# Kernel tuning notes

Hardware: AMD Instinct MI355X
Metric: run time of the kernel (lower is better)

The kernel has to match this reference:

```python
import jax, jax.numpy as jnp
import numpy as np

V_NUM = 4
NUM_HEADS = 8


def setup_inputs() -> dict:
    key = jax.random.key(0)
    k1, k2, k3 = jax.random.split(key, 3)
    B, C, H, W = 8, 512, 24, 24
    x = jax.random.normal(k1, (B, C, H, W), dtype=jnp.float32)
    # 1x1 conv weights stored as [out_ch, in_ch]
    w_qkv = jax.random.normal(k2, (3 * C, C), dtype=jnp.float32) * (C ** -0.5)
    w_proj = jax.random.normal(k3, (C, C), dtype=jnp.float32) * (C ** -0.5)
    b_proj = jnp.zeros((C,), dtype=jnp.float32)
    return {"x": x, "w_qkv": w_qkv, "w_proj": w_proj, "b_proj": b_proj}


def reference(x, w_qkv, w_proj, b_proj):
    B, C, H, W = x.shape
    hd = C // NUM_HEADS          # head dim
    scale = hd ** -0.5
    g = B // V_NUM               # batch groups
    N = V_NUM * H * W            # tokens per group

    # 1x1 conv qkv (no bias): [B, 3C, H, W]
    qkv = jnp.einsum('bchw,oc->bohw', x, w_qkv)
    # [g, v, 3C, H, W] -> [g, 3C, v, H, W] -> [g, heads, 3*hd, N]
    t = qkv.reshape(g, V_NUM, 3 * C, H, W).transpose(0, 2, 1, 3, 4)
    t = t.reshape(g, NUM_HEADS, 3 * hd, N)
    q, k, v = jnp.split(t, 3, axis=2)  # each [g, heads, hd, N]

    # attn = k^T @ q * scale : [g, heads, N, N]
    attn = jnp.einsum('ghdn,ghdm->ghnm', k, q) * scale
    attn = jax.nn.softmax(attn, axis=-2)  # softmax over the k axis (dim=-2)

    # out = v @ attn : [g, heads, hd, N]
    out = jnp.einsum('ghdn,ghnm->ghdm', v, attn)
    # [g, C, v, H, W] -> [g, v, C, H, W] -> [B, C, H, W]
    out = out.reshape(g, C, V_NUM, H, W).transpose(0, 2, 1, 3, 4).reshape(B, C, H, W)

    # 1x1 conv proj with bias
    out = jnp.einsum('bchw,oc->bohw', out, w_proj) + b_proj[None, :, None, None]
    return out
```

## Files before the change

kernel.cpp:

```cpp
#include <hip/hip_runtime.h>
#include <stdint.h>

typedef _Float16 f16;
typedef _Float16 half8 __attribute__((ext_vector_type(8)));
typedef _Float16 half4 __attribute__((ext_vector_type(4)));
typedef float floatx4 __attribute__((ext_vector_type(4)));

#define LOG2E 1.44269504088896340736f

__device__ __forceinline__ void async_cp16(const void* g, void* l) {
  __builtin_amdgcn_global_load_lds((const __attribute__((address_space(1))) void*)g,
                                   (__attribute__((address_space(3))) void*)l, 16, 0, 0);
}

__global__ __launch_bounds__(256) void k_prep(const float* __restrict__ x,
                                              f16* __restrict__ XT,
                                              const float* __restrict__ wqkv,
                                              const float* __restrict__ wproj,
                                              f16* __restrict__ WQ, f16* __restrict__ WP) {
  __shared__ f16 sT[64][72];
  const int bid = blockIdx.x;
  const int tid = threadIdx.x;
  if (bid < 576) {
    const int hw0 = (bid % 9) * 64, c0 = ((bid / 9) & 7) * 64, b = bid / 72;
    const int cc = tid >> 6, hwc = tid & 63;
    const float* xb = x + (size_t)b * 294912;
    for (int i = 0; i < 16; ++i) {
      int c = c0 + i * 4 + cc;
      sT[hwc][i * 4 + cc] = (f16)xb[c * 576 + hw0 + hwc];
    }
    __syncthreads();
    const int c_c = tid & 63, rr = tid >> 6;
    f16* xtb = XT + ((size_t)b * 576 + hw0) * 512 + c0;
    for (int j = 0; j < 16; ++j) {
      int r = j * 4 + rr;
      xtb[(size_t)r * 512 + c_c] = sT[r][c_c];
    }
  } else {
    const float SCALE_Q = 0.125f * LOG2E;
    const int total1 = 1536 * 512, total2 = 512 * 512;
    for (int idx = (bid - 576) * 256 + tid; idx < total1 + total2; idx += 128 * 256) {
      if (idx < total1) {
        int row = idx >> 9;
        float v = wqkv[idx];
        if ((row % 192) < 64) v *= SCALE_Q;
        WQ[idx] = (f16)v;
      } else {
        WP[idx - total1] = (f16)wproj[idx - total1];
      }
    }
  }
}

__global__ __launch_bounds__(256) void k_qkv_gemm(const f16* __restrict__ XT,
                                                  const f16* __restrict__ WQ,
                                                  f16* __restrict__ Qh, f16* __restrict__ Kh,
                                                  f16* __restrict__ Vh) {
  const int t0 = blockIdx.x * 128, n0 = blockIdx.y * 128;
  __shared__ alignas(16) f16 smem[2 * 128 * 64];
  f16* sA = smem;
  f16* sB = smem + 128 * 64;
  const int tid = threadIdx.x;
  const int wave = tid >> 6, lane = tid & 63, quad = lane >> 4, l16 = lane & 15;
  const int msub = (wave & 1) * 64, nsub = (wave >> 1) * 64;
  const floatx4 fzero = {0.f, 0.f, 0.f, 0.f};
  floatx4 acc[4][4];
  for (int i = 0; i < 4; ++i)
    for (int j = 0; j < 4; ++j) acc[i][j] = fzero;

  for (int k0 = 0; k0 < 512; k0 += 64) {
    __syncthreads();
    for (int p = 0; p < 4; ++p) {
      int e = p * 256 + tid;
      int row = e >> 3, colb = e & 7;
      async_cp16((const char*)XT + ((size_t)(t0 + row) * 512 + k0 + colb * 8) * 2,
                 (char*)sA + e * 16);
      async_cp16((const char*)WQ + ((size_t)(n0 + row) * 512 + k0 + colb * 8) * 2,
                 (char*)sB + e * 16);
    }
    __syncthreads();
    for (int f = 0; f < 2; ++f) {
      half8 a[4], bfr[4];
      for (int ms = 0; ms < 4; ++ms)
        a[ms] = *(const half8*)&sA[(msub + ms * 16 + l16) * 64 + f * 32 + quad * 8];
      for (int ns = 0; ns < 4; ++ns)
        bfr[ns] = *(const half8*)&sB[(nsub + ns * 16 + l16) * 64 + f * 32 + quad * 8];
      for (int ms = 0; ms < 4; ++ms)
        for (int ns = 0; ns < 4; ++ns)
          acc[ms][ns] =
              __builtin_amdgcn_mfma_f32_16x16x32_f16(a[ms], bfr[ns], acc[ms][ns], 0, 0, 0);
    }
  }
  for (int ms = 0; ms < 4; ++ms) {
    int tbase = t0 + msub + ms * 16 + quad * 4;
    for (int ns = 0; ns < 4; ++ns) {
      int row = n0 + nsub + ns * 16 + l16;
      int h = row / 192, rr2 = row % 192;
      int sel = rr2 >> 6, d = rr2 & 63;
      if (sel == 2) continue;
      for (int r = 0; r < 4; ++r) {
        int t = tbase + r;
        int b = t / 576, hw = t % 576;
        int g = b >> 2, v = b & 3;
        int n = v * 576 + hw;
        int gh = g * 8 + h;
        f16 hv = (f16)acc[ms][ns][r];
        size_t idx = ((size_t)gh * 2304 + n) * 64 + d;
        if (sel == 0)
          Qh[idx] = hv;
        else
          Kh[idx] = hv;
      }
    }
  }
  const int r0 = n0 % 192;
  if (r0 != 0) {
    const int vloc = (r0 == 128) ? 0 : 64;
    const int h = (n0 + vloc) / 192;
    f16* sVT = smem;
    __syncthreads();
    if ((wave >> 1) == (vloc >> 6)) {
      for (int ms = 0; ms < 4; ++ms) {
        int tok = msub + ms * 16 + quad * 4;
        for (int ns = 0; ns < 4; ++ns) {
          int d = ns * 16 + l16;
          half4 hv;
          for (int r = 0; r < 4; ++r) hv[r] = (f16)acc[ms][ns][r];
          *(half4*)&sVT[d * 136 + tok] = hv;
        }
      }
    }
    __syncthreads();
    for (int pss = 0; pss < 4; ++pss) {
      int d = pss * 16 + (tid >> 4), chunk = tid & 15;
      int t = t0 + chunk * 8;
      int b = t / 576, hw = t - b * 576;
      int gh = (b >> 2) * 8 + h, n = (b & 3) * 576 + hw;
      *(half8*)(Vh + (size_t)gh * 147456 + (size_t)d * 2304 + n) =
          *(const half8*)&sVT[d * 136 + chunk * 8];
    }
  }
}

__global__ __launch_bounds__(256) void k_attn(const f16* __restrict__ Qh,
                                              const f16* __restrict__ Kh,
                                              const f16* __restrict__ Vh,
                                              f16* __restrict__ AOT) {
  const int mt = blockIdx.x, gh = blockIdx.y;
  const int m0 = mt * 64;
  const int g = gh >> 3, h = gh & 7;
  const f16* Qg = Qh + (size_t)gh * 147456;
  const f16* Kg = Kh + (size_t)gh * 147456;
  const f16* Vg = Vh + (size_t)gh * 147456;
  __shared__ alignas(16) f16 sK[2][2][64 * 64];
  __shared__ alignas(16) f16 sV[2][2][64 * 64];
  const int tid = threadIdx.x;
  const int wave = tid >> 6, lane = tid & 63, quad = lane >> 4, l16 = lane & 15;
  const int wq = wave & 1, half = wave >> 1;
  const floatx4 fzero = {0.f, 0.f, 0.f, 0.f};
  const int sw = l16 & 7;

  auto stage_kv = [&](int ktile, int buf) {
#pragma unroll
    for (int p = 0; p < 8; ++p) {
      const int half_t = (p >> 1) & 1, isV = p >> 2;
      int idx = (p & 1) * 256 + tid;
      int row = idx >> 3, cb = idx & 7, sc = ((cb ^ (row & 7)) << 3);
      int nb = half_t * 1152 + ktile * 64;
      if (!isV)
        async_cp16(Kg + (size_t)(nb + row) * 64 + sc, (char*)&sK[half_t][buf][0] + idx * 16);
      else
        async_cp16(Vg + (size_t)row * 2304 + nb + sc, (char*)&sV[half_t][buf][0] + idx * 16);
    }
  };

  half8 qa[2][2];
  for (int s = 0; s < 2; ++s) {
    int qrow = m0 + wq * 32 + s * 16 + l16;
    qa[s][0] = *(const half8*)(Qg + (size_t)qrow * 64 + quad * 8);
    qa[s][1] = *(const half8*)(Qg + (size_t)qrow * 64 + 32 + quad * 8);
  }

  stage_kv(0, 0);
  __syncthreads();
  stage_kv(1, 1);

  float l_lane[2] = {0.f, 0.f};
  floatx4 o[2][4];
  for (int s = 0; s < 2; ++s)
    for (int dt = 0; dt < 4; ++dt) o[s][dt] = fzero;

  for (int kt = 0; kt < 18; ++kt) {
    const f16* bK = &sK[half][kt & 1][0];
    const f16* bV = &sV[half][kt & 1][0];

    half4 pf[2][4];
#pragma unroll
    for (int nt = 0; nt < 4; ++nt) {
      int krow = nt * 16 + l16;
      half8 kb0 = *(const half8*)&bK[krow * 64 + ((quad ^ sw) << 3)];
      half8 kb1 = *(const half8*)&bK[krow * 64 + (((4 + quad) ^ sw) << 3)];
#pragma unroll
      for (int s = 0; s < 2; ++s) {
        floatx4 t = __builtin_amdgcn_mfma_f32_16x16x32_f16(kb0, qa[s][0], fzero, 0, 0, 0);
        t = __builtin_amdgcn_mfma_f32_16x16x32_f16(kb1, qa[s][1], t, 0, 0, 0);
#pragma unroll
        for (int r = 0; r < 4; ++r) {
          float e = __builtin_amdgcn_exp2f(t[r]);
          l_lane[s] += e;
          pf[s][nt][r] = (f16)e;
        }
      }
    }
#pragma unroll
    for (int dt = 0; dt < 4; ++dt) {
      int vrow = dt * 16 + l16;
#pragma unroll
      for (int nt = 0; nt < 4; ++nt) {
        int chunk = nt * 2 + (quad >> 1);
        half4 vb = *(const half4*)&bV[vrow * 64 + ((chunk ^ sw) << 3) + (quad & 1) * 4];
#pragma unroll
        for (int s = 0; s < 2; ++s)
          o[s][dt] = __builtin_amdgcn_mfma_f32_16x16x16f16(pf[s][nt], vb, o[s][dt], 0, 0, 0);
      }
    }

    if (kt < 17) {
      __syncthreads();
      if (kt + 2 < 18) stage_kv(kt + 2, kt & 1);
    }
  }

  __syncthreads();
  float* cO = (float*)sK;
  float* cL = (float*)sV;
  if (half == 1) {
    for (int s = 0; s < 2; ++s) {
      cL[(wq * 2 + s) * 64 + lane] = l_lane[s];
      for (int dt = 0; dt < 4; ++dt)
        *(floatx4*)&cO[((((wq * 2 + s) * 4 + dt) * 64 + lane) * 4)] = o[s][dt];
    }
  }
  __syncthreads();
  if (half == 0) {
    for (int s = 0; s < 2; ++s) {
      l_lane[s] += cL[(wq * 2 + s) * 64 + lane];
      for (int dt = 0; dt < 4; ++dt)
        o[s][dt] += *(const floatx4*)&cO[((((wq * 2 + s) * 4 + dt) * 64 + lane) * 4)];
    }
    for (int s = 0; s < 2; ++s) {
      l_lane[s] += __shfl_xor(l_lane[s], 16, 64);
      l_lane[s] += __shfl_xor(l_lane[s], 32, 64);
      float inv[4];
      for (int r = 0; r < 4; ++r) {
        float lr = __shfl(l_lane[s], quad * 4 + r, 64);
        inv[r] = 1.f / lr;
      }
      for (int dt = 0; dt < 4; ++dt)
        for (int r = 0; r < 4; ++r) {
          int n_tok = m0 + wq * 32 + s * 16 + quad * 4 + r;
          int v = n_tok / 576, hw = n_tok % 576;
          int bb = g * 4 + v;
          int c = h * 64 + dt * 16 + l16;
          AOT[((size_t)bb * 576 + hw) * 512 + c] = (f16)(o[s][dt][r] * inv[r]);
        }
    }
  }
}

__global__ __launch_bounds__(256) void k_proj_gemm(const f16* __restrict__ AOT,
                                                   const f16* __restrict__ WP,
                                                   const float* __restrict__ bias,
                                                   float* __restrict__ out) {
  const int o0 = blockIdx.x * 64, t0 = blockIdx.y * 128;
  __shared__ alignas(16) f16 sA[64 * 64];
  __shared__ alignas(16) f16 sB[128 * 64];
  const int tid = threadIdx.x;
  const int wave = tid >> 6, lane = tid & 63, quad = lane >> 4, l16 = lane & 15;
  const int msub = (wave & 1) * 32, nsub = (wave >> 1) * 64;
  const floatx4 fzero = {0.f, 0.f, 0.f, 0.f};
  floatx4 acc[2][4];
  for (int i = 0; i < 2; ++i)
    for (int j = 0; j < 4; ++j) acc[i][j] = fzero;

  for (int k0 = 0; k0 < 512; k0 += 64) {
    __syncthreads();
    for (int p = 0; p < 2; ++p) {
      int e = p * 256 + tid;
      int row = e >> 3, colb = e & 7;
      async_cp16((const char*)WP + ((size_t)(o0 + row) * 512 + k0 + colb * 8) * 2,
                 (char*)sA + e * 16);
    }
    for (int p = 0; p < 4; ++p) {
      int e = p * 256 + tid;
      int row = e >> 3, colb = e & 7;
      async_cp16((const char*)AOT + ((size_t)(t0 + row) * 512 + k0 + colb * 8) * 2,
                 (char*)sB + e * 16);
    }
    __syncthreads();
    for (int f = 0; f < 2; ++f) {
      half8 a[2], bfr[4];
      for (int ms = 0; ms < 2; ++ms)
        a[ms] = *(const half8*)&sA[(msub + ms * 16 + l16) * 64 + f * 32 + quad * 8];
      for (int ns = 0; ns < 4; ++ns)
        bfr[ns] = *(const half8*)&sB[(nsub + ns * 16 + l16) * 64 + f * 32 + quad * 8];
      for (int ms = 0; ms < 2; ++ms)
        for (int ns = 0; ns < 4; ++ns)
          acc[ms][ns] =
              __builtin_amdgcn_mfma_f32_16x16x32_f16(a[ms], bfr[ns], acc[ms][ns], 0, 0, 0);
    }
  }
  for (int ms = 0; ms < 2; ++ms) {
    int o_row = o0 + msub + ms * 16 + quad * 4;
    for (int ns = 0; ns < 4; ++ns) {
      int t = t0 + nsub + ns * 16 + l16;
      int b = t / 576, hw = t % 576;
      for (int r = 0; r < 4; ++r) {
        int orow = o_row + r;
        out[(size_t)b * 294912 + (size_t)orow * 576 + hw] = acc[ms][ns][r] + bias[orow];
      }
    }
  }
}

extern "C" void kernel_launch(void* const* d_in, const int* in_sizes, int n_in,
                              void* d_out, int out_size, void* d_ws, size_t ws_size,
                              hipStream_t stream) {
  const float* x = (const float*)d_in[0];
  const float* wqkv = (const float*)d_in[1];
  const float* wproj = (const float*)d_in[2];
  const float* bias = (const float*)d_in[3];
  float* out = (float*)d_out;
  char* ws = (char*)d_ws;
  f16* XT = (f16*)(ws + 0);
  f16* WQ = (f16*)(ws + 4718592);
  f16* WP = (f16*)(ws + 6291456);
  f16* Qh = (f16*)(ws + 6815744);
  f16* Kh = (f16*)(ws + 11534336);
  f16* Vh = (f16*)(ws + 16252928);
  f16* AOT = (f16*)(ws + 20971520);

  k_prep<<<dim3(704), dim3(256), 0, stream>>>(x, XT, wqkv, wproj, WQ, WP);
  k_qkv_gemm<<<dim3(36, 12), dim3(256), 0, stream>>>(XT, WQ, Qh, Kh, Vh);
  k_attn<<<dim3(36, 16), dim3(256), 0, stream>>>(Qh, Kh, Vh, AOT);
  k_proj_gemm<<<dim3(8, 36), dim3(256), 0, stream>>>(AOT, WP, bias, out);
}
```

Before: 154.9 us.

## Split attention key range across blocks with global partials and reduction kernel

```diff
diff --git a/kernel.cpp b/kernel.cpp
--- a/kernel.cpp
+++ b/kernel.cpp
@@ -142,6 +142,139 @@
   }
 }
 
+__global__ __launch_bounds__(128) void k_attn_part(const f16* __restrict__ Qh,
+                                                   const f16* __restrict__ Kh,
+                                                   const f16* __restrict__ Vh,
+                                                   float* __restrict__ Opart,
+                                                   float* __restrict__ Lpart) {
+  const int mt = blockIdx.x, gh = blockIdx.y, ks = blockIdx.z;
+  const int m0 = mt * 64;
+  const f16* Qg = Qh + (size_t)gh * 147456;
+  const f16* Kg = Kh + (size_t)gh * 147456 + (size_t)ks * 73728;
+  const f16* Vg = Vh + (size_t)gh * 147456 + ks * 1152;
+  __shared__ alignas(16) f16 sK[2][64 * 64];
+  __shared__ alignas(16) f16 sV[2][64 * 64];
+  const int tid = threadIdx.x;
+  const int wave = tid >> 6, lane = tid & 63, quad = lane >> 4, l16 = lane & 15;
+  const floatx4 fzero = {0.f, 0.f, 0.f, 0.f};
+  const int sw = l16 & 7;
+
+  auto stage_kv = [&](int ktile, int buf) {
+    const int nb = ktile * 64;
+#pragma unroll
+    for (int p = 0; p < 4; ++p) {
+      int idx = p * 128 + tid;
+      int row = idx >> 3, cb = idx & 7, sc = ((cb ^ (row & 7)) << 3);
+      async_cp16(Kg + (size_t)(nb + row) * 64 + sc, (char*)&sK[buf][0] + idx * 16);
+    }
+#pragma unroll
+    for (int p = 0; p < 4; ++p) {
+      int idx = p * 128 + tid;
+      int row = idx >> 3, cb = idx & 7, sc = ((cb ^ (row & 7)) << 3);
+      async_cp16(Vg + (size_t)row * 2304 + nb + sc, (char*)&sV[buf][0] + idx * 16);
+    }
+  };
+
+  half8 qa[2][2];
+  for (int s = 0; s < 2; ++s) {
+    int qrow = m0 + wave * 32 + s * 16 + l16;
+    qa[s][0] = *(const half8*)(Qg + (size_t)qrow * 64 + quad * 8);
+    qa[s][1] = *(const half8*)(Qg + (size_t)qrow * 64 + 32 + quad * 8);
+  }
+
+  stage_kv(0, 0);
+  __syncthreads();
+  stage_kv(1, 1);
+
+  float l_lane[2] = {0.f, 0.f};
+  floatx4 o[2][4];
+  for (int s = 0; s < 2; ++s)
+    for (int dt = 0; dt < 4; ++dt) o[s][dt] = fzero;
+
+  for (int kt = 0; kt < 18; ++kt) {
+    const f16* bK = &sK[kt & 1][0];
+    const f16* bV = &sV[kt & 1][0];
+
+    half4 pf[2][4];
+#pragma unroll
+    for (int nt = 0; nt < 4; ++nt) {
+      int krow = nt * 16 + l16;
+      half8 kb0 = *(const half8*)&bK[krow * 64 + ((quad ^ sw) << 3)];
+      half8 kb1 = *(const half8*)&bK[krow * 64 + (((4 + quad) ^ sw) << 3)];
+#pragma unroll
+      for (int s = 0; s < 2; ++s) {
+        floatx4 t = __builtin_amdgcn_mfma_f32_16x16x32_f16(kb0, qa[s][0], fzero, 0, 0, 0);
+        t = __builtin_amdgcn_mfma_f32_16x16x32_f16(kb1, qa[s][1], t, 0, 0, 0);
+#pragma unroll
+        for (int r = 0; r < 4; ++r) {
+          float e = __builtin_amdgcn_exp2f(t[r]);
+          l_lane[s] += e;
+          pf[s][nt][r] = (f16)e;
+        }
+      }
+    }
+#pragma unroll
+    for (int dt = 0; dt < 4; ++dt) {
+      int vrow = dt * 16 + l16;
+#pragma unroll
+      for (int nt = 0; nt < 4; ++nt) {
+        int chunk = nt * 2 + (quad >> 1);
+        half4 vb = *(const half4*)&bV[vrow * 64 + ((chunk ^ sw) << 3) + (quad & 1) * 4];
+#pragma unroll
+        for (int s = 0; s < 2; ++s)
+          o[s][dt] = __builtin_amdgcn_mfma_f32_16x16x16f16(pf[s][nt], vb, o[s][dt], 0, 0, 0);
+      }
+    }
+
+    if (kt < 17) {
+      __syncthreads();
+      if (kt + 2 < 18) stage_kv(kt + 2, kt & 1);
+    }
+  }
+
+  const size_t slice = (size_t)(ks * 16 + gh);
+  for (int s = 0; s < 2; ++s) {
+    l_lane[s] += __shfl_xor(l_lane[s], 16, 64);
+    l_lane[s] += __shfl_xor(l_lane[s], 32, 64);
+    if (quad == 0)
+      Lpart[slice * 2304 + m0 + wave * 32 + s * 16 + l16] = l_lane[s];
+  }
+  float* Ob = Opart + slice * (2304 * 64);
+  for (int s = 0; s < 2; ++s)
+    for (int dt = 0; dt < 4; ++dt)
+      for (int r = 0; r < 4; ++r) {
+        int q = m0 + wave * 32 + s * 16 + quad * 4 + r;
+        Ob[(size_t)q * 64 + dt * 16 + l16] = o[s][dt][r];
+      }
+}
+
+__global__ __launch_bounds__(256) void k_attn_red(const float* __restrict__ Opart,
+                                                  const float* __restrict__ Lpart,
+                                                  f16* __restrict__ AOT) {
+  const int mt = blockIdx.x, gh = blockIdx.y;
+  const int g = gh >> 3, h = gh & 7;
+  const int tid = threadIdx.x;
+  const int q = mt * 64 + (tid >> 2), dseg = (tid & 3) * 16;
+  const size_t s0 = (size_t)gh, s1 = (size_t)(16 + gh);
+  float l = Lpart[s0 * 2304 + q] + Lpart[s1 * 2304 + q];
+  float inv = 1.f / l;
+  const float* O0 = Opart + (s0 * 2304 + q) * 64 + dseg;
+  const float* O1 = Opart + (s1 * 2304 + q) * 64 + dseg;
+  int v = q / 576, hw = q % 576;
+  int bb = g * 4 + v;
+  f16* dst = AOT + ((size_t)bb * 576 + hw) * 512 + h * 64 + dseg;
+  for (int p = 0; p < 2; ++p) {
+    floatx4 a = *(const floatx4*)(O0 + p * 8);
+    floatx4 b = *(const floatx4*)(O1 + p * 8);
+    floatx4 a2 = *(const floatx4*)(O0 + p * 8 + 4);
+    floatx4 b2 = *(const floatx4*)(O1 + p * 8 + 4);
+    half8 hv;
+    for (int j = 0; j < 4; ++j) hv[j] = (f16)((a[j] + b[j]) * inv);
+    for (int j = 0; j < 4; ++j) hv[4 + j] = (f16)((a2[j] + b2[j]) * inv);
+    *(half8*)(dst + p * 8) = hv;
+  }
+}
+
 __global__ __launch_bounds__(256) void k_attn(const f16* __restrict__ Qh,
                                               const f16* __restrict__ Kh,
                                               const f16* __restrict__ Vh,
@@ -193,7 +326,6 @@
   for (int kt = 0; kt < 18; ++kt) {
     const f16* bK = &sK[half][kt & 1][0];
     const f16* bV = &sV[half][kt & 1][0];
-
     half4 pf[2][4];
 #pragma unroll
     for (int nt = 0; nt < 4; ++nt) {
@@ -224,7 +356,6 @@
           o[s][dt] = __builtin_amdgcn_mfma_f32_16x16x16f16(pf[s][nt], vb, o[s][dt], 0, 0, 0);
       }
     }
-
     if (kt < 17) {
       __syncthreads();
       if (kt + 2 < 18) stage_kv(kt + 2, kt & 1);
@@ -339,9 +470,18 @@
   f16* Kh = (f16*)(ws + 11534336);
   f16* Vh = (f16*)(ws + 16252928);
   f16* AOT = (f16*)(ws + 20971520);
+  float* Opart = (float*)(ws + 25690112);
+  float* Lpart = (float*)(ws + 44564480);
+
+  const bool two_pass = (ws_size >= 44859392u);
 
   k_prep<<<dim3(704), dim3(256), 0, stream>>>(x, XT, wqkv, wproj, WQ, WP);
   k_qkv_gemm<<<dim3(36, 12), dim3(256), 0, stream>>>(XT, WQ, Qh, Kh, Vh);
-  k_attn<<<dim3(36, 16), dim3(256), 0, stream>>>(Qh, Kh, Vh, AOT);
+  if (two_pass) {
+    k_attn_part<<<dim3(36, 16, 2), dim3(128), 0, stream>>>(Qh, Kh, Vh, Opart, Lpart);
+    k_attn_red<<<dim3(36, 16), dim3(256), 0, stream>>>(Opart, Lpart, AOT);
+  } else {
+    k_attn<<<dim3(36, 16), dim3(256), 0, stream>>>(Qh, Kh, Vh, AOT);
+  }
   k_proj_gemm<<<dim3(8, 36), dim3(256), 0, stream>>>(AOT, WP, bias, out);
 }
```

Measured after the change: 167.0 us. 7.8% more time.

## Load K/V straight to registers in attention, dropping LDS staging and split-K

Applied to the files above, without the earlier changes.

```diff
diff --git a/kernel.cpp b/kernel.cpp
--- a/kernel.cpp
+++ b/kernel.cpp
@@ -147,63 +147,55 @@
                                               const f16* __restrict__ Vh,
                                               f16* __restrict__ AOT) {
   const int mt = blockIdx.x, gh = blockIdx.y;
-  const int m0 = mt * 64;
   const int g = gh >> 3, h = gh & 7;
   const f16* Qg = Qh + (size_t)gh * 147456;
   const f16* Kg = Kh + (size_t)gh * 147456;
   const f16* Vg = Vh + (size_t)gh * 147456;
-  __shared__ alignas(16) f16 sK[2][2][64 * 64];
-  __shared__ alignas(16) f16 sV[2][2][64 * 64];
   const int tid = threadIdx.x;
   const int wave = tid >> 6, lane = tid & 63, quad = lane >> 4, l16 = lane & 15;
-  const int wq = wave & 1, half = wave >> 1;
+  const int m0 = mt * 128 + wave * 32;
   const floatx4 fzero = {0.f, 0.f, 0.f, 0.f};
-  const int sw = l16 & 7;
-
-  auto stage_kv = [&](int ktile, int buf) {
-#pragma unroll
-    for (int p = 0; p < 8; ++p) {
-      const int half_t = (p >> 1) & 1, isV = p >> 2;
-      int idx = (p & 1) * 256 + tid;
-      int row = idx >> 3, cb = idx & 7, sc = ((cb ^ (row & 7)) << 3);
-      int nb = half_t * 1152 + ktile * 64;
-      if (!isV)
-        async_cp16(Kg + (size_t)(nb + row) * 64 + sc, (char*)&sK[half_t][buf][0] + idx * 16);
-      else
-        async_cp16(Vg + (size_t)row * 2304 + nb + sc, (char*)&sV[half_t][buf][0] + idx * 16);
-    }
-  };
 
   half8 qa[2][2];
+#pragma unroll
   for (int s = 0; s < 2; ++s) {
-    int qrow = m0 + wq * 32 + s * 16 + l16;
+    int qrow = m0 + s * 16 + l16;
     qa[s][0] = *(const half8*)(Qg + (size_t)qrow * 64 + quad * 8);
     qa[s][1] = *(const half8*)(Qg + (size_t)qrow * 64 + 32 + quad * 8);
   }
 
-  stage_kv(0, 0);
-  __syncthreads();
-  stage_kv(1, 1);
+  half8 kb[2][4][2];
+  half4 vb[2][4][4];
+
+  auto load_tile = [&](int n0, half8 (&k)[4][2], half4 (&v)[4][4]) {
+#pragma unroll
+    for (int nt = 0; nt < 4; ++nt) {
+      const f16* kr = Kg + (size_t)(n0 + nt * 16 + l16) * 64 + quad * 8;
+      k[nt][0] = *(const half8*)kr;
+      k[nt][1] = *(const half8*)(kr + 32);
+    }
+#pragma unroll
+    for (int dt = 0; dt < 4; ++dt) {
+      const f16* vr = Vg + (size_t)(dt * 16 + l16) * 2304 + n0 + quad * 4;
+#pragma unroll
+      for (int nt = 0; nt < 4; ++nt) v[dt][nt] = *(const half4*)(vr + nt * 16);
+    }
+  };
 
   float l_lane[2] = {0.f, 0.f};
   floatx4 o[2][4];
+#pragma unroll
   for (int s = 0; s < 2; ++s)
     for (int dt = 0; dt < 4; ++dt) o[s][dt] = fzero;
 
-  for (int kt = 0; kt < 18; ++kt) {
-    const f16* bK = &sK[half][kt & 1][0];
-    const f16* bV = &sV[half][kt & 1][0];
-
+  auto compute = [&](const half8 (&k)[4][2], const half4 (&v)[4][4]) {
     half4 pf[2][4];
 #pragma unroll
     for (int nt = 0; nt < 4; ++nt) {
-      int krow = nt * 16 + l16;
-      half8 kb0 = *(const half8*)&bK[krow * 64 + ((quad ^ sw) << 3)];
-      half8 kb1 = *(const half8*)&bK[krow * 64 + (((4 + quad) ^ sw) << 3)];
 #pragma unroll
       for (int s = 0; s < 2; ++s) {
-        floatx4 t = __builtin_amdgcn_mfma_f32_16x16x32_f16(kb0, qa[s][0], fzero, 0, 0, 0);
-        t = __builtin_amdgcn_mfma_f32_16x16x32_f16(kb1, qa[s][1], t, 0, 0, 0);
+        floatx4 t = __builtin_amdgcn_mfma_f32_16x16x32_f16(k[nt][0], qa[s][0], fzero, 0, 0, 0);
+        t = __builtin_amdgcn_mfma_f32_16x16x32_f16(k[nt][1], qa[s][1], t, 0, 0, 0);
 #pragma unroll
         for (int r = 0; r < 4; ++r) {
           float e = __builtin_amdgcn_exp2f(t[r]);
@@ -213,58 +205,42 @@
       }
     }
 #pragma unroll
-    for (int dt = 0; dt < 4; ++dt) {
-      int vrow = dt * 16 + l16;
-#pragma unroll
-      for (int nt = 0; nt < 4; ++nt) {
-        int chunk = nt * 2 + (quad >> 1);
-        half4 vb = *(const half4*)&bV[vrow * 64 + ((chunk ^ sw) << 3) + (quad & 1) * 4];
+    for (int dt = 0; dt < 4; ++dt)
+#pragma unroll
+      for (int nt = 0; nt < 4; ++nt)
 #pragma unroll
         for (int s = 0; s < 2; ++s)
-          o[s][dt] = __builtin_amdgcn_mfma_f32_16x16x16f16(pf[s][nt], vb, o[s][dt], 0, 0, 0);
-      }
-    }
-
-    if (kt < 17) {
-      __syncthreads();
-      if (kt + 2 < 18) stage_kv(kt + 2, kt & 1);
-    }
-  }
-
-  __syncthreads();
-  float* cO = (float*)sK;
-  float* cL = (float*)sV;
-  if (half == 1) {
-    for (int s = 0; s < 2; ++s) {
-      cL[(wq * 2 + s) * 64 + lane] = l_lane[s];
-      for (int dt = 0; dt < 4; ++dt)
-        *(floatx4*)&cO[((((wq * 2 + s) * 4 + dt) * 64 + lane) * 4)] = o[s][dt];
-    }
-  }
-  __syncthreads();
-  if (half == 0) {
-    for (int s = 0; s < 2; ++s) {
-      l_lane[s] += cL[(wq * 2 + s) * 64 + lane];
-      for (int dt = 0; dt < 4; ++dt)
-        o[s][dt] += *(const floatx4*)&cO[((((wq * 2 + s) * 4 + dt) * 64 + lane) * 4)];
-    }
-    for (int s = 0; s < 2; ++s) {
-      l_lane[s] += __shfl_xor(l_lane[s], 16, 64);
-      l_lane[s] += __shfl_xor(l_lane[s], 32, 64);
-      float inv[4];
+          o[s][dt] = __builtin_amdgcn_mfma_f32_16x16x16f16(pf[s][nt], v[dt][nt], o[s][dt], 0, 0, 0);
+  };
+
+  load_tile(0, kb[0], vb[0]);
+  for (int kt = 0; kt < 36; kt += 2) {
+    load_tile((kt + 1) * 64, kb[1], vb[1]);
+    compute(kb[0], vb[0]);
+    if (kt + 2 < 36) load_tile((kt + 2) * 64, kb[0], vb[0]);
+    compute(kb[1], vb[1]);
+  }
+
+#pragma unroll
+  for (int s = 0; s < 2; ++s) {
+    l_lane[s] += __shfl_xor(l_lane[s], 16, 64);
+    l_lane[s] += __shfl_xor(l_lane[s], 32, 64);
+    float inv[4];
+#pragma unroll
+    for (int r = 0; r < 4; ++r) {
+      float lr = __shfl(l_lane[s], quad * 4 + r, 64);
+      inv[r] = 1.f / lr;
+    }
+#pragma unroll
+    for (int dt = 0; dt < 4; ++dt)
+#pragma unroll
       for (int r = 0; r < 4; ++r) {
-        float lr = __shfl(l_lane[s], quad * 4 + r, 64);
-        inv[r] = 1.f / lr;
-      }
-      for (int dt = 0; dt < 4; ++dt)
-        for (int r = 0; r < 4; ++r) {
-          int n_tok = m0 + wq * 32 + s * 16 + quad * 4 + r;
-          int v = n_tok / 576, hw = n_tok % 576;
-          int bb = g * 4 + v;
-          int c = h * 64 + dt * 16 + l16;
-          AOT[((size_t)bb * 576 + hw) * 512 + c] = (f16)(o[s][dt][r] * inv[r]);
-        }
-    }
+        int n_tok = m0 + s * 16 + quad * 4 + r;
+        int v = n_tok / 576, hw = n_tok % 576;
+        int bb = g * 4 + v;
+        int c = h * 64 + dt * 16 + l16;
+        AOT[((size_t)bb * 576 + hw) * 512 + c] = (f16)(o[s][dt][r] * inv[r]);
+      }
   }
 }
 
@@ -342,6 +318,6 @@
 
   k_prep<<<dim3(704), dim3(256), 0, stream>>>(x, XT, wqkv, wproj, WQ, WP);
   k_qkv_gemm<<<dim3(36, 12), dim3(256), 0, stream>>>(XT, WQ, Qh, Kh, Vh);
-  k_attn<<<dim3(36, 16), dim3(256), 0, stream>>>(Qh, Kh, Vh, AOT);
+  k_attn<<<dim3(18, 16), dim3(256), 0, stream>>>(Qh, Kh, Vh, AOT);
   k_proj_gemm<<<dim3(8, 36), dim3(256), 0, stream>>>(AOT, WP, bias, out);
 }
```

Result: slower. 298.3 us (+92.6%).
